# Optimization experiments

Hardware: AMD Instinct MI355X
Metric: run time of the kernel (lower is better)

Reference implementation:

```python
import jax, jax.numpy as jnp
import numpy as np

B, T, D_IN, D_OUT = 4, 2048, 1024, 1024

def setup_inputs() -> dict:
    key = jax.random.key(0)
    k1, k2, k3, k4 = jax.random.split(key, 4)
    scale = 0.02
    return {
        "x": jax.random.normal(k1, (B, T, D_IN), dtype=jnp.float32),
        "W_query": jax.random.normal(k2, (D_IN, D_OUT), dtype=jnp.float32) * scale,
        "W_key": jax.random.normal(k3, (D_IN, D_OUT), dtype=jnp.float32) * scale,
        "W_value": jax.random.normal(k4, (D_IN, D_OUT), dtype=jnp.float32) * scale,
    }

def reference(x, W_query, W_key, W_value):
    # QKV projections (Linear without bias)
    q = jnp.einsum("btd,de->bte", x, W_query)
    k = jnp.einsum("btd,de->bte", x, W_key)
    v = jnp.einsum("btd,de->bte", x, W_value)
    num_tokens = x.shape[1]
    d_out = k.shape[-1]
    # raw scores [B, T, T]
    scores = jnp.einsum("bqd,bkd->bqk", q, k)
    # causal mask: position q may attend to k <= q
    causal = jnp.tril(jnp.ones((num_tokens, num_tokens), dtype=bool))
    scores = jnp.where(causal, scores, -jnp.inf)
    attn = jax.nn.softmax(scores / jnp.sqrt(jnp.float32(d_out)), axis=-1)
    # dropout is identity at eval / p=0.0
    context = jnp.einsum("bqk,bkd->bqd", attn, v)
    return context
```

## Files before the change

kernel.cpp:

```cpp
#include <hip/hip_runtime.h>
#include <hip/hip_bf16.h>
#include <stdint.h>

typedef short short8 __attribute__((ext_vector_type(8)));
typedef short short4v __attribute__((ext_vector_type(4)));
typedef float f32x4 __attribute__((ext_vector_type(4)));

__device__ __forceinline__ void gload16(const void* g, void* l) {
  __builtin_amdgcn_global_load_lds((const __attribute__((address_space(1))) void*)g,
                                   (__attribute__((address_space(3))) void*)l, 16, 0, 0);
}

__device__ __forceinline__ unsigned short f2b(float f) {
  unsigned int x = __float_as_uint(f);
  x += 0x7fffu + ((x >> 16) & 1u);
  return (unsigned short)(x >> 16);
}

__global__ __launch_bounds__(256) void prep(
    const float* __restrict__ x, const float* __restrict__ Wq,
    const float* __restrict__ Wk, const float* __restrict__ Wv,
    unsigned short* __restrict__ xb, unsigned short* __restrict__ Wt2,
    float* __restrict__ sums)
{
  __shared__ __align__(16) char smem[16384];
  const int bid = blockIdx.x;
  const int tid = threadIdx.x;
  if (bid < 8192) {
    const int i = bid * 256 + tid;
    const float4 f = ((const float4*)x)[i];
    union { unsigned short u[4]; uint2 v; } o;
    o.u[0] = f2b(f.x); o.u[1] = f2b(f.y); o.u[2] = f2b(f.z); o.u[3] = f2b(f.w);
    ((uint2*)xb)[i] = o.v;
  } else if (bid < 9216) {
    float (*tb)[33] = (float(*)[33])smem;
    const int t = bid - 8192;
    const int bx = t & 31, by = t >> 5;
    const int tx = tid & 31, ty = tid >> 5;
    const int xcol = bx * 32 + tx, y0 = by * 32;
    #pragma unroll
    for (int i = 0; i < 4; ++i)
      tb[ty + i * 8][tx] = Wv[(long long)(y0 + ty + i * 8) * 1024 + xcol];
    __syncthreads();
    unsigned short* O = Wt2 + 1024 * 1024;
    const int xo = by * 32 + tx, yo0 = bx * 32;
    #pragma unroll
    for (int i = 0; i < 4; ++i)
      O[(long long)(yo0 + ty + i * 8) * 1024 + xo] = f2b(tb[tx][ty + i * 8]);
  } else if (bid < 9472) {
    const int t = bid - 9216;
    const int bx = t & 15, by = t >> 4;
    const int row0 = by * 64, col0 = bx * 64;
    const int wave = tid >> 6, lane = tid & 63;
    const int wr = wave >> 1, wc = wave & 1;
    const int l15 = lane & 15, lk = lane >> 4;
    const int sr = lane >> 3, sg = lane & 7;
    char* lA = smem;
    char* lB = smem + 8192;
    const int rA = wr * 32 + l15, cB = wc * 32 + l15;
    const int xorA = (rA & 7) << 4, xorB = (cB & 7) << 4;
    const int kb = lk * 16;
    f32x4 acc[2][2];
    #pragma unroll
    for (int m = 0; m < 2; ++m)
      #pragma unroll
      for (int n = 0; n < 2; ++n) acc[m][n] = (f32x4)0.0f;
    for (int kt = 0; kt < 16; ++kt) {
      const int kc = kt * 64;
      short8 va[2], vb[2];
      int rr[2];
      #pragma unroll
      for (int j = 0; j < 2; ++j) {
        const int ci = wave * 2 + j;
        const int r = ci * 8 + sr;
        rr[j] = r;
        const float* pa = Wk + (long long)(row0 + r) * 1024 + kc + sg * 8;
        const float* pb = Wq + (long long)(col0 + r) * 1024 + kc + sg * 8;
        const float4 a0 = *(const float4*)pa, a1 = *(const float4*)(pa + 4);
        const float4 b0 = *(const float4*)pb, b1 = *(const float4*)(pb + 4);
        va[j][0] = (short)f2b(a0.x); va[j][1] = (short)f2b(a0.y);
        va[j][2] = (short)f2b(a0.z); va[j][3] = (short)f2b(a0.w);
        va[j][4] = (short)f2b(a1.x); va[j][5] = (short)f2b(a1.y);
        va[j][6] = (short)f2b(a1.z); va[j][7] = (short)f2b(a1.w);
        vb[j][0] = (short)f2b(b0.x); vb[j][1] = (short)f2b(b0.y);
        vb[j][2] = (short)f2b(b0.z); vb[j][3] = (short)f2b(b0.w);
        vb[j][4] = (short)f2b(b1.x); vb[j][5] = (short)f2b(b1.y);
        vb[j][6] = (short)f2b(b1.z); vb[j][7] = (short)f2b(b1.w);
      }
      __syncthreads();
      #pragma unroll
      for (int j = 0; j < 2; ++j) {
        const int off = rr[j] * 128 + ((sg * 16) ^ ((rr[j] & 7) << 4));
        *(short8*)(lA + off) = va[j];
        *(short8*)(lB + off) = vb[j];
      }
      __syncthreads();
      #pragma unroll
      for (int ks = 0; ks < 2; ++ks) {
        short8 af[2], bf[2];
        #pragma unroll
        for (int m = 0; m < 2; ++m)
          af[m] = *(const short8*)(lA + (rA + m * 16) * 128 + ((ks * 64 + kb) ^ xorA));
        #pragma unroll
        for (int n = 0; n < 2; ++n)
          bf[n] = *(const short8*)(lB + (cB + n * 16) * 128 + ((ks * 64 + kb) ^ xorB));
        #pragma unroll
        for (int m = 0; m < 2; ++m)
          #pragma unroll
          for (int n = 0; n < 2; ++n)
            acc[m][n] = __builtin_amdgcn_mfma_f32_16x16x32_bf16(af[m], bf[n], acc[m][n], 0, 0, 0);
      }
    }
    const int orow = row0 + wr * 32 + lk * 4;
    const int ocol = col0 + wc * 32 + l15;
    #pragma unroll
    for (int m = 0; m < 2; ++m)
      #pragma unroll
      for (int r = 0; r < 4; ++r)
        #pragma unroll
        for (int n = 0; n < 2; ++n)
          Wt2[(long long)(orow + m * 16 + r) * 1024 + ocol + n * 16] = f2b(acc[m][n][r]);
  } else {
    const int i = (bid - 9472) * 256 + tid;
    sums[i] = 0.f;
  }
}

#define STG(buf, isB, half, kt) do {                                           \
    const unsigned short* _s = (isB) ? Bz : Az;                                \
    const int _ld = (isB) ? ldb : lda;                                         \
    const int _b0 = (isB) ? col0 : row0;                                       \
    char* _d = lds + (buf) * 65536 + (isB) * 32768 + (half) * 16384;           \
    _Pragma("unroll")                                                          \
    for (int _i = 0; _i < 2; ++_i) {                                           \
      const int _c = wave * 2 + _i;                                            \
      const int _row = (half) * 128 + _c * 8 + srow;                           \
      gload16(_s + (long long)(_b0 + _row) * _ld + (kt) * 64 + sgrp * 8,       \
              _d + _c * 1024);                                                 \
    } } while (0)

#define LDA8(dst, buf, mh) do {                                                \
    _Pragma("unroll")                                                          \
    for (int _m = 0; _m < 4; ++_m) {                                           \
      const int _r = wr * 128 + ((mh) * 4 + _m) * 16 + (lane & 15);            \
      const char* _p = lds + (buf) * 65536 + _r * 128;                         \
      const int _x = (_r & 7) << 4;                                            \
      dst[_m][0] = *(const short8*)(_p + ((kbyte) ^ _x));                      \
      dst[_m][1] = *(const short8*)(_p + ((64 + kbyte) ^ _x));                 \
    } } while (0)

#define LDB4(dst, buf, nh) do {                                                \
    _Pragma("unroll")                                                          \
    for (int _n = 0; _n < 2; ++_n) {                                           \
      const int _r = wc * 64 + ((nh) * 2 + _n) * 16 + (lane & 15);             \
      const char* _p = lds + (buf) * 65536 + 32768 + _r * 128;                 \
      const int _x = (_r & 7) << 4;                                            \
      dst[_n][0] = *(const short8*)(_p + ((kbyte) ^ _x));                      \
      dst[_n][1] = *(const short8*)(_p + ((64 + kbyte) ^ _x));                 \
    } } while (0)

#define MFMA16(mh, nh, av, bv) do {                                            \
    __builtin_amdgcn_s_setprio(1);                                             \
    _Pragma("unroll") for (int _n = 0; _n < 2; ++_n)                           \
    _Pragma("unroll") for (int _m = 0; _m < 4; ++_m)                           \
    _Pragma("unroll") for (int _k = 0; _k < 2; ++_k)                           \
      acc[(mh)*4+_m][(nh)*2+_n] = __builtin_amdgcn_mfma_f32_16x16x32_bf16(     \
          av[_m][_k], bv[_n][_k], acc[(mh)*4+_m][(nh)*2+_n], 0, 0, 0);         \
    __builtin_amdgcn_s_setprio(0);                                             \
  } while (0)

#define BAR() __builtin_amdgcn_s_barrier()
#define VM4() asm volatile("s_waitcnt vmcnt(4)" ::: "memory")
#define VM0() asm volatile("s_waitcnt vmcnt(0)" ::: "memory")

#define GEMM8_BODY(NT)                                                         \
  f32x4 acc[8][4];                                                             \
  _Pragma("unroll")                                                            \
  for (int m = 0; m < 8; ++m)                                                  \
    _Pragma("unroll")                                                          \
    for (int n = 0; n < 4; ++n) acc[m][n] = (f32x4)0.0f;                       \
  short8 a[4][2], b0[2][2], b1[2][2];                                          \
  STG(0, 1, 0, 0); STG(0, 1, 1, 0); STG(0, 0, 0, 0); STG(0, 0, 1, 0);          \
  STG(1, 1, 0, 1); STG(1, 1, 1, 1);                                            \
  VM4(); BAR();                                                                \
  for (int t = 0; t < (NT); ++t) {                                             \
    const bool pf = (t < (NT) - 1);                                            \
    LDA8(a, 0, 0); LDB4(b0, 0, 0);                                             \
    STG(1, 0, 0, 2 * t + 1);                                                   \
    BAR(); MFMA16(0, 0, a, b0); BAR();                                         \
    LDB4(b1, 0, 1);                                                            \
    STG(1, 0, 1, 2 * t + 1);                                                   \
    BAR(); MFMA16(0, 1, a, b1); BAR();                                         \
    LDA8(a, 0, 1);                                                             \
    if (pf) STG(0, 1, 0, 2 * t + 2);                                           \
    BAR(); MFMA16(1, 1, a, b1); BAR();                                         \
    if (pf) STG(0, 1, 1, 2 * t + 2);                                           \
    BAR(); MFMA16(1, 0, a, b0);                                                \
    if (pf) VM4(); else VM0();                                                 \
    BAR();                                                                     \
    LDA8(a, 1, 0); LDB4(b0, 1, 0);                                             \
    if (pf) STG(0, 0, 0, 2 * t + 2);                                           \
    BAR(); MFMA16(0, 0, a, b0); BAR();                                         \
    LDB4(b1, 1, 1);                                                            \
    if (pf) STG(0, 0, 1, 2 * t + 2);                                           \
    BAR(); MFMA16(0, 1, a, b1); BAR();                                         \
    LDA8(a, 1, 1);                                                             \
    if (pf) STG(1, 1, 0, 2 * t + 3);                                           \
    BAR(); MFMA16(1, 1, a, b1); BAR();                                         \
    if (pf) STG(1, 1, 1, 2 * t + 3);                                           \
    BAR(); MFMA16(1, 0, a, b0);                                                \
    if (pf) VM4();                                                             \
    BAR();                                                                     \
  }

__global__ __launch_bounds__(512, 2) void gemm8_yv(
    const unsigned short* __restrict__ A, const unsigned short* __restrict__ Bt,
    unsigned short* __restrict__ y, unsigned short* __restrict__ vt)
{
  const int row0 = blockIdx.y * 256;
  const int col0 = blockIdx.x * 256;
  const unsigned short* Az = A;
  const unsigned short* Bz = Bt;
  const int lda = 1024, ldb = 1024;

  __shared__ __align__(16) char lds[131072];

  const int tid = threadIdx.x;
  const int wave = tid >> 6, lane = tid & 63;
  const int wr = wave >> 2, wc = wave & 3;
  const int srow = lane >> 3, sgrp = (lane & 7) ^ srow;
  const int kbyte = (lane >> 4) * 16;

  GEMM8_BODY(8)

  const int orow = row0 + wr * 128 + ((lane >> 4) << 2);
  const int ocol = col0 + wc * 64 + (lane & 15);
  if (col0 < 1024) {
    #pragma unroll
    for (int m = 0; m < 8; ++m)
      #pragma unroll
      for (int r = 0; r < 4; ++r) {
        const int rg = orow + m * 16 + r;
        #pragma unroll
        for (int n = 0; n < 4; ++n)
          y[(long long)rg * 1024 + ocol + n * 16] = f2b(acc[m][n][r]);
      }
  } else {
    const int b = row0 >> 11;
    const int t0 = (row0 & 2047) + wr * 128 + ((lane >> 4) << 2);
    const int d0 = (col0 - 1024) + wc * 64 + (lane & 15);
    #pragma unroll
    for (int n = 0; n < 4; ++n) {
      unsigned short* vrow = vt + ((long long)b * 1024 + d0 + n * 16) * 2048 + t0;
      #pragma unroll
      for (int m = 0; m < 8; ++m) {
        short4v v;
        v[0] = (short)f2b(acc[m][n][0]);
        v[1] = (short)f2b(acc[m][n][1]);
        v[2] = (short)f2b(acc[m][n][2]);
        v[3] = (short)f2b(acc[m][n][3]);
        *(short4v*)(vrow + m * 16) = v;
      }
    }
  }
}

__global__ __launch_bounds__(512, 2) void gemm8_p(
    const unsigned short* __restrict__ A, const unsigned short* __restrict__ Bt,
    unsigned short* __restrict__ outp, float* __restrict__ sums)
{
  const int z = blockIdx.z;
  const int row0 = blockIdx.y * 256;
  const int col0 = blockIdx.x * 256;
  if (col0 > row0 + 255) return;

  const unsigned short* Az = A + (long long)z * (2048 * 1024);
  const unsigned short* Bz = Bt + (long long)z * (2048 * 1024);
  const int lda = 1024, ldb = 1024;

  __shared__ __align__(16) char lds[131072];

  const int tid = threadIdx.x;
  const int wave = tid >> 6, lane = tid & 63;
  const int wr = wave >> 2, wc = wave & 3;
  const int srow = lane >> 3, sgrp = (lane & 7) ^ srow;
  const int kbyte = (lane >> 4) * 16;

  GEMM8_BODY(8)

  const int orow = row0 + wr * 128 + ((lane >> 4) << 2);
  const int ocol = col0 + wc * 64 + (lane & 15);
  unsigned short* out = outp + (long long)z * (2048 * 2048);
  #pragma unroll
  for (int m = 0; m < 8; ++m)
    #pragma unroll
    for (int r = 0; r < 4; ++r) {
      const int rg = orow + m * 16 + r;
      float rs = 0.f;
      #pragma unroll
      for (int n = 0; n < 4; ++n) {
        const int cg = ocol + n * 16;
        float p = (cg > rg) ? 0.0f : __expf(acc[m][n][r] * 0.03125f);
        rs += p;
        out[(long long)rg * 2048 + cg] = f2b(p);
      }
      #pragma unroll
      for (int off = 1; off < 16; off <<= 1) rs += __shfl_xor(rs, off);
      if ((lane & 15) == 0) atomicAdd(&sums[(long long)z * 2048 + rg], rs);
    }
}

__global__ __launch_bounds__(256) void gemm_pv(
    const unsigned short* __restrict__ P, const unsigned short* __restrict__ Vt,
    float* __restrict__ out, const float* __restrict__ sums)
{
  const int z = blockIdx.z;
  const int row0 = (15 - blockIdx.y) * 128;
  const int col0 = blockIdx.x * 128;

  const unsigned short* Az = P + (long long)z * (2048 * 2048);
  const unsigned short* Bz = Vt + (long long)z * (1024 * 2048);

  __shared__ __align__(16) char lds[32768];

  const int tid = threadIdx.x;
  const int wave = tid >> 6;
  const int lane = tid & 63;
  const int wr = wave >> 1, wc = wave & 1;
  const int l15 = lane & 15, lk = lane >> 4;

  const int srow = lane >> 3;
  const int sgrp = (lane & 7) ^ srow;

  const int rA = wr * 64 + l15;
  const int cB = wc * 64 + l15;
  const int kb = lk * 16;
  const int xorA = (rA & 7) << 4;
  const int xorB = (cB & 7) << 4;

  f32x4 acc[4][4];
  #pragma unroll
  for (int m = 0; m < 4; ++m)
    #pragma unroll
    for (int n = 0; n < 4; ++n) acc[m][n] = (f32x4)0.0f;

  const int nkt = (row0 + 128) >> 6;

  for (int kt = 0; kt < nkt; ++kt) {
    const int kc = kt * 64;
    #pragma unroll
    for (int i = 0; i < 4; ++i) {
      const int ci = wave * 4 + i;
      gload16(Az + (long long)(row0 + ci * 8 + srow) * 2048 + kc + sgrp * 8,
              lds + ci * 1024);
      gload16(Bz + (long long)(col0 + ci * 8 + srow) * 2048 + kc + sgrp * 8,
              lds + 16384 + ci * 1024);
    }
    __syncthreads();
    #pragma unroll
    for (int ks = 0; ks < 2; ++ks) {
      short8 af[4], bfr[4];
      #pragma unroll
      for (int m = 0; m < 4; ++m)
        af[m] = *(const short8*)(lds + (rA + m * 16) * 128 + ((ks * 64 + kb) ^ xorA));
      #pragma unroll
      for (int n = 0; n < 4; ++n)
        bfr[n] = *(const short8*)(lds + 16384 + (cB + n * 16) * 128 + ((ks * 64 + kb) ^ xorB));
      #pragma unroll
      for (int m = 0; m < 4; ++m)
        #pragma unroll
        for (int n = 0; n < 4; ++n)
          acc[m][n] = __builtin_amdgcn_mfma_f32_16x16x32_bf16(af[m], bfr[n], acc[m][n], 0, 0, 0);
    }
    __syncthreads();
  }

  const int orow = row0 + wr * 64 + lk * 4;
  const int ocol = col0 + wc * 64 + l15;
  const float* sz = sums + (long long)z * 2048;
  float* oz = out + (long long)z * (2048 * 1024);
  #pragma unroll
  for (int m = 0; m < 4; ++m)
    #pragma unroll
    for (int r = 0; r < 4; ++r) {
      const int rg = orow + m * 16 + r;
      const float iv = 1.0f / sz[rg];
      #pragma unroll
      for (int n = 0; n < 4; ++n)
        oz[(long long)rg * 1024 + ocol + n * 16] = acc[m][n][r] * iv;
    }
}

extern "C" void kernel_launch(void* const* d_in, const int* in_sizes, int n_in,
                              void* d_out, int out_size, void* d_ws, size_t ws_size,
                              hipStream_t stream) {
  (void)in_sizes; (void)n_in; (void)out_size; (void)ws_size;
  const float* x  = (const float*)d_in[0];
  const float* Wq = (const float*)d_in[1];
  const float* Wk = (const float*)d_in[2];
  const float* Wv = (const float*)d_in[3];
  float* out = (float*)d_out;

  char* ws = (char*)d_ws;
  unsigned short* xb  = (unsigned short*)(ws);
  unsigned short* Wt2 = (unsigned short*)(ws + 16777216);
  unsigned short* y   = (unsigned short*)(ws + 20971520);
  unsigned short* Vt  = (unsigned short*)(ws + 37748736);
  unsigned short* P   = (unsigned short*)(ws + 54525952);
  float*          sums = (float*)(ws + 88080384);

  prep<<<9504, 256, 0, stream>>>(x, Wq, Wk, Wv, xb, Wt2, sums);

  gemm8_yv<<<dim3(8, 32), 512, 0, stream>>>(xb, Wt2, y, Vt);

  gemm8_p<<<dim3(8, 8, 4), 512, 0, stream>>>(y, xb, P, sums);

  gemm_pv<<<dim3(8, 16, 4), 256, 0, stream>>>(P, Vt, out, sums);
}
```

Before: 156.7 us.

## Unify score and PV GEMMs into triangular-scheduled 256x128 kernel with split-K

Replaces the score GEMM and the PV GEMM with one templated 256x128-tile kernel. The score mode enumerates only lower-triangular tiles through a flattened index, so no blocks launch just to exit early. The PV mode splits the long K range of the bottom four row blocks into two halves that atomically add into the output, which is pre-zeroed for those rows by extra blocks in prep. This balances per-block work across the causal triangle and gives PV the deeper pipelined schedule, at the cost of float atomics, more prep work and narrower tiles.

```diff
diff --git a/kernel.cpp b/kernel.cpp
--- a/kernel.cpp
+++ b/kernel.cpp
@@ -21,7 +21,7 @@
     const float* __restrict__ x, const float* __restrict__ Wq,
     const float* __restrict__ Wk, const float* __restrict__ Wv,
     unsigned short* __restrict__ xb, unsigned short* __restrict__ Wt2,
-    float* __restrict__ sums)
+    float* __restrict__ sums, float* __restrict__ out)
 {
   __shared__ __align__(16) char smem[16384];
   const int bid = blockIdx.x;
@@ -120,9 +120,15 @@
         #pragma unroll
         for (int n = 0; n < 2; ++n)
           Wt2[(long long)(orow + m * 16 + r) * 1024 + ocol + n * 16] = f2b(acc[m][n][r]);
-  } else {
+  } else if (bid < 9504) {
     const int i = (bid - 9472) * 256 + tid;
     sums[i] = 0.f;
+  } else {
+    const long long i = (long long)(bid - 9504) * 256 + tid;
+    const int z = (int)(i >> 18);
+    const int r = (int)(i & 262143);
+    float4* p = (float4*)(out + (long long)z * 2097152 + 1048576) + r;
+    *p = make_float4(0.f, 0.f, 0.f, 0.f);
   }
 }
 
@@ -171,47 +177,8 @@
 
 #define BAR() __builtin_amdgcn_s_barrier()
 #define VM4() asm volatile("s_waitcnt vmcnt(4)" ::: "memory")
+#define VM2() asm volatile("s_waitcnt vmcnt(2)" ::: "memory")
 #define VM0() asm volatile("s_waitcnt vmcnt(0)" ::: "memory")
-
-#define GEMM8_BODY(NT)                                                         \
-  f32x4 acc[8][4];                                                             \
-  _Pragma("unroll")                                                            \
-  for (int m = 0; m < 8; ++m)                                                  \
-    _Pragma("unroll")                                                          \
-    for (int n = 0; n < 4; ++n) acc[m][n] = (f32x4)0.0f;                       \
-  short8 a[4][2], b0[2][2], b1[2][2];                                          \
-  STG(0, 1, 0, 0); STG(0, 1, 1, 0); STG(0, 0, 0, 0); STG(0, 0, 1, 0);          \
-  STG(1, 1, 0, 1); STG(1, 1, 1, 1);                                            \
-  VM4(); BAR();                                                                \
-  for (int t = 0; t < (NT); ++t) {                                             \
-    const bool pf = (t < (NT) - 1);                                            \
-    LDA8(a, 0, 0); LDB4(b0, 0, 0);                                             \
-    STG(1, 0, 0, 2 * t + 1);                                                   \
-    BAR(); MFMA16(0, 0, a, b0); BAR();                                         \
-    LDB4(b1, 0, 1);                                                            \
-    STG(1, 0, 1, 2 * t + 1);                                                   \
-    BAR(); MFMA16(0, 1, a, b1); BAR();                                         \
-    LDA8(a, 0, 1);                                                             \
-    if (pf) STG(0, 1, 0, 2 * t + 2);                                           \
-    BAR(); MFMA16(1, 1, a, b1); BAR();                                         \
-    if (pf) STG(0, 1, 1, 2 * t + 2);                                           \
-    BAR(); MFMA16(1, 0, a, b0);                                                \
-    if (pf) VM4(); else VM0();                                                 \
-    BAR();                                                                     \
-    LDA8(a, 1, 0); LDB4(b0, 1, 0);                                             \
-    if (pf) STG(0, 0, 0, 2 * t + 2);                                           \
-    BAR(); MFMA16(0, 0, a, b0); BAR();                                         \
-    LDB4(b1, 1, 1);                                                            \
-    if (pf) STG(0, 0, 1, 2 * t + 2);                                           \
-    BAR(); MFMA16(0, 1, a, b1); BAR();                                         \
-    LDA8(a, 1, 1);                                                             \
-    if (pf) STG(1, 1, 0, 2 * t + 3);                                           \
-    BAR(); MFMA16(1, 1, a, b1); BAR();                                         \
-    if (pf) STG(1, 1, 1, 2 * t + 3);                                           \
-    BAR(); MFMA16(1, 0, a, b0);                                                \
-    if (pf) VM4();                                                             \
-    BAR();                                                                     \
-  }
 
 __global__ __launch_bounds__(512, 2) void gemm8_yv(
     const unsigned short* __restrict__ A, const unsigned short* __restrict__ Bt,
@@ -230,8 +197,48 @@
   const int wr = wave >> 2, wc = wave & 3;
   const int srow = lane >> 3, sgrp = (lane & 7) ^ srow;
   const int kbyte = (lane >> 4) * 16;
-
-  GEMM8_BODY(8)
+  const int nt = 8;
+
+  f32x4 acc[8][4];
+  #pragma unroll
+  for (int m = 0; m < 8; ++m)
+    #pragma unroll
+    for (int n = 0; n < 4; ++n) acc[m][n] = (f32x4)0.0f;
+  short8 a[4][2], b0[2][2], b1[2][2];
+
+  STG(0, 1, 0, 0); STG(0, 1, 1, 0); STG(0, 0, 0, 0); STG(0, 0, 1, 0);
+  STG(1, 1, 0, 1); STG(1, 1, 1, 1);
+  VM4(); BAR();
+
+  for (int t = 0; t < nt; ++t) {
+    const bool pf = (t < nt - 1);
+    LDA8(a, 0, 0); LDB4(b0, 0, 0);
+    STG(1, 0, 0, 2 * t + 1);
+    BAR(); MFMA16(0, 0, a, b0); BAR();
+    LDB4(b1, 0, 1);
+    STG(1, 0, 1, 2 * t + 1);
+    BAR(); MFMA16(0, 1, a, b1); BAR();
+    LDA8(a, 0, 1);
+    if (pf) STG(0, 1, 0, 2 * t + 2);
+    BAR(); MFMA16(1, 1, a, b1); BAR();
+    if (pf) STG(0, 1, 1, 2 * t + 2);
+    BAR(); MFMA16(1, 0, a, b0);
+    if (pf) VM4(); else VM0();
+    BAR();
+    LDA8(a, 1, 0); LDB4(b0, 1, 0);
+    if (pf) STG(0, 0, 0, 2 * t + 2);
+    BAR(); MFMA16(0, 0, a, b0); BAR();
+    LDB4(b1, 1, 1);
+    if (pf) STG(0, 0, 1, 2 * t + 2);
+    BAR(); MFMA16(0, 1, a, b1); BAR();
+    LDA8(a, 1, 1);
+    if (pf) STG(1, 1, 0, 2 * t + 3);
+    BAR(); MFMA16(1, 1, a, b1); BAR();
+    if (pf) STG(1, 1, 1, 2 * t + 3);
+    BAR(); MFMA16(1, 0, a, b0);
+    if (pf) VM4();
+    BAR();
+  }
 
   const int orow = row0 + wr * 128 + ((lane >> 4) << 2);
   const int ocol = col0 + wc * 64 + (lane & 15);
@@ -265,20 +272,92 @@
   }
 }
 
-__global__ __launch_bounds__(512, 2) void gemm8_p(
-    const unsigned short* __restrict__ A, const unsigned short* __restrict__ Bt,
-    unsigned short* __restrict__ outp, float* __restrict__ sums)
+#define STGA2(buf, half, kt) do {                                              \
+    _Pragma("unroll")                                                          \
+    for (int _i = 0; _i < 2; ++_i) {                                           \
+      const int _c = wave * 2 + _i;                                            \
+      gload16(Az + (long long)(row0 + (half) * 128 + _c * 8 + srow) * lda +    \
+                  (kt) * 64 + sgrp * 8,                                        \
+              lds + (buf) * 32768 + (half) * 16384 + _c * 1024);               \
+    } } while (0)
+
+#define STGB2(buf, half, kt)                                                   \
+    gload16(Bz + (long long)(col0 + (half) * 64 + wave * 8 + srow) * ldb +     \
+                (kt) * 64 + sgrp * 8,                                          \
+            lds + 65536 + (buf) * 16384 + (half) * 8192 + wave * 1024)
+
+#define LDA8N(dst, buf, mh) do {                                               \
+    _Pragma("unroll")                                                          \
+    for (int _m = 0; _m < 4; ++_m) {                                           \
+      const int _r = wr * 128 + ((mh) * 4 + _m) * 16 + (lane & 15);            \
+      const char* _p = lds + (buf) * 32768 + _r * 128;                         \
+      const int _x = (_r & 7) << 4;                                            \
+      dst[_m][0] = *(const short8*)(_p + ((kbyte) ^ _x));                      \
+      dst[_m][1] = *(const short8*)(_p + ((64 + kbyte) ^ _x));                 \
+    } } while (0)
+
+#define LDB1N(dst, buf, nf) do {                                               \
+    const int _r = wc * 32 + (nf) * 16 + (lane & 15);                          \
+    const char* _p = lds + 65536 + (buf) * 16384 + _r * 128;                   \
+    const int _x = (_r & 7) << 4;                                              \
+    dst[0] = *(const short8*)(_p + ((kbyte) ^ _x));                            \
+    dst[1] = *(const short8*)(_p + ((64 + kbyte) ^ _x));                       \
+  } while (0)
+
+#define MFMA8N(mh, nf, av, bv) do {                                            \
+    __builtin_amdgcn_s_setprio(1);                                             \
+    _Pragma("unroll") for (int _m = 0; _m < 4; ++_m)                           \
+    _Pragma("unroll") for (int _k = 0; _k < 2; ++_k)                           \
+      acc[(mh)*4+_m][nf] = __builtin_amdgcn_mfma_f32_16x16x32_bf16(            \
+          av[_m][_k], bv[_k], acc[(mh)*4+_m][nf], 0, 0, 0);                    \
+    __builtin_amdgcn_s_setprio(0);                                             \
+  } while (0)
+
+template<int MODE>
+__global__ __launch_bounds__(512, 2) void gemm8n(
+    const unsigned short* __restrict__ Abase, const unsigned short* __restrict__ Bbase,
+    void* __restrict__ outv, float* __restrict__ sums)
 {
   const int z = blockIdx.z;
-  const int row0 = blockIdx.y * 256;
-  const int col0 = blockIdx.x * 256;
-  if (col0 > row0 + 255) return;
-
-  const unsigned short* Az = A + (long long)z * (2048 * 1024);
-  const unsigned short* Bz = Bt + (long long)z * (2048 * 1024);
-  const int lda = 1024, ldb = 1024;
-
-  __shared__ __align__(16) char lds[131072];
+  const int f = blockIdx.x;
+  int row0, col0, k0, nt;
+  bool atomic = false;
+  const unsigned short *Az, *Bz;
+  int lda, ldb;
+
+  if (MODE == 1) {
+    int by = (int)((sqrtf(4.f * f + 1.f) - 1.f) * 0.5f);
+    while (by * (by + 1) > f) --by;
+    while ((by + 1) * (by + 2) <= f) ++by;
+    const int bx = f - by * (by + 1);
+    row0 = by * 256; col0 = bx * 128; k0 = 0; nt = 8;
+    Az = Abase + (long long)z * (2048 * 1024);
+    Bz = Bbase + (long long)z * (2048 * 1024);
+    lda = 1024; ldb = 1024;
+  } else {
+    int by, bx;
+    if (f < 64) {
+      by = 7 - (f >> 4);
+      const int c = (f >> 3) & 1;
+      bx = f & 7;
+      k0 = c * 1024;
+      const int kEnd = 256 * (by + 1);
+      nt = ((c == 0 ? 1024 : kEnd - 1024) >> 7);
+      atomic = true;
+    } else {
+      const int g = f - 64;
+      by = 3 - (g >> 3);
+      bx = g & 7;
+      k0 = 0;
+      nt = (256 * (by + 1)) >> 7;
+    }
+    row0 = by * 256; col0 = bx * 128;
+    Az = Abase + (long long)z * (2048 * 2048) + k0;
+    Bz = Bbase + (long long)z * (1024 * 2048) + k0;
+    lda = 2048; ldb = 2048;
+  }
+
+  __shared__ __align__(16) char lds[98304];
 
   const int tid = threadIdx.x;
   const int wave = tid >> 6, lane = tid & 63;
@@ -286,109 +365,84 @@
   const int srow = lane >> 3, sgrp = (lane & 7) ^ srow;
   const int kbyte = (lane >> 4) * 16;
 
-  GEMM8_BODY(8)
+  f32x4 acc[8][2];
+  #pragma unroll
+  for (int m = 0; m < 8; ++m) { acc[m][0] = (f32x4)0.0f; acc[m][1] = (f32x4)0.0f; }
+  short8 a[4][2], b0[2], b1[2];
+
+  STGB2(0, 0, 0); STGB2(0, 1, 0); STGA2(0, 0, 0); STGA2(0, 1, 0);
+  STGB2(1, 0, 1); STGB2(1, 1, 1);
+  VM2(); BAR();
+
+  for (int t = 0; t < nt; ++t) {
+    const bool pf = (t < nt - 1);
+    LDA8N(a, 0, 0); LDB1N(b0, 0, 0);
+    STGA2(1, 0, 2 * t + 1);
+    BAR(); MFMA8N(0, 0, a, b0); BAR();
+    LDB1N(b1, 0, 1);
+    STGA2(1, 1, 2 * t + 1);
+    BAR(); MFMA8N(0, 1, a, b1); BAR();
+    LDA8N(a, 0, 1);
+    if (pf) STGB2(0, 0, 2 * t + 2);
+    BAR(); MFMA8N(1, 1, a, b1); BAR();
+    if (pf) STGB2(0, 1, 2 * t + 2);
+    BAR(); MFMA8N(1, 0, a, b0);
+    if (pf) VM2(); else VM0();
+    BAR();
+    LDA8N(a, 1, 0); LDB1N(b0, 1, 0);
+    if (pf) STGA2(0, 0, 2 * t + 2);
+    BAR(); MFMA8N(0, 0, a, b0); BAR();
+    LDB1N(b1, 1, 1);
+    if (pf) STGA2(0, 1, 2 * t + 2);
+    BAR(); MFMA8N(0, 1, a, b1); BAR();
+    LDA8N(a, 1, 1);
+    if (pf) STGB2(1, 0, 2 * t + 3);
+    BAR(); MFMA8N(1, 1, a, b1); BAR();
+    if (pf) STGB2(1, 1, 2 * t + 3);
+    BAR(); MFMA8N(1, 0, a, b0);
+    if (pf) VM2();
+    BAR();
+  }
 
   const int orow = row0 + wr * 128 + ((lane >> 4) << 2);
-  const int ocol = col0 + wc * 64 + (lane & 15);
-  unsigned short* out = outp + (long long)z * (2048 * 2048);
-  #pragma unroll
-  for (int m = 0; m < 8; ++m)
-    #pragma unroll
-    for (int r = 0; r < 4; ++r) {
-      const int rg = orow + m * 16 + r;
-      float rs = 0.f;
-      #pragma unroll
-      for (int n = 0; n < 4; ++n) {
-        const int cg = ocol + n * 16;
-        float p = (cg > rg) ? 0.0f : __expf(acc[m][n][r] * 0.03125f);
-        rs += p;
-        out[(long long)rg * 2048 + cg] = f2b(p);
-      }
-      #pragma unroll
-      for (int off = 1; off < 16; off <<= 1) rs += __shfl_xor(rs, off);
-      if ((lane & 15) == 0) atomicAdd(&sums[(long long)z * 2048 + rg], rs);
-    }
-}
-
-__global__ __launch_bounds__(256) void gemm_pv(
-    const unsigned short* __restrict__ P, const unsigned short* __restrict__ Vt,
-    float* __restrict__ out, const float* __restrict__ sums)
-{
-  const int z = blockIdx.z;
-  const int row0 = (15 - blockIdx.y) * 128;
-  const int col0 = blockIdx.x * 128;
-
-  const unsigned short* Az = P + (long long)z * (2048 * 2048);
-  const unsigned short* Bz = Vt + (long long)z * (1024 * 2048);
-
-  __shared__ __align__(16) char lds[32768];
-
-  const int tid = threadIdx.x;
-  const int wave = tid >> 6;
-  const int lane = tid & 63;
-  const int wr = wave >> 1, wc = wave & 1;
-  const int l15 = lane & 15, lk = lane >> 4;
-
-  const int srow = lane >> 3;
-  const int sgrp = (lane & 7) ^ srow;
-
-  const int rA = wr * 64 + l15;
-  const int cB = wc * 64 + l15;
-  const int kb = lk * 16;
-  const int xorA = (rA & 7) << 4;
-  const int xorB = (cB & 7) << 4;
-
-  f32x4 acc[4][4];
-  #pragma unroll
-  for (int m = 0; m < 4; ++m)
-    #pragma unroll
-    for (int n = 0; n < 4; ++n) acc[m][n] = (f32x4)0.0f;
-
-  const int nkt = (row0 + 128) >> 6;
-
-  for (int kt = 0; kt < nkt; ++kt) {
-    const int kc = kt * 64;
-    #pragma unroll
-    for (int i = 0; i < 4; ++i) {
-      const int ci = wave * 4 + i;
-      gload16(Az + (long long)(row0 + ci * 8 + srow) * 2048 + kc + sgrp * 8,
-              lds + ci * 1024);
-      gload16(Bz + (long long)(col0 + ci * 8 + srow) * 2048 + kc + sgrp * 8,
-              lds + 16384 + ci * 1024);
-    }
-    __syncthreads();
-    #pragma unroll
-    for (int ks = 0; ks < 2; ++ks) {
-      short8 af[4], bfr[4];
-      #pragma unroll
-      for (int m = 0; m < 4; ++m)
-        af[m] = *(const short8*)(lds + (rA + m * 16) * 128 + ((ks * 64 + kb) ^ xorA));
-      #pragma unroll
-      for (int n = 0; n < 4; ++n)
-        bfr[n] = *(const short8*)(lds + 16384 + (cB + n * 16) * 128 + ((ks * 64 + kb) ^ xorB));
-      #pragma unroll
-      for (int m = 0; m < 4; ++m)
-        #pragma unroll
-        for (int n = 0; n < 4; ++n)
-          acc[m][n] = __builtin_amdgcn_mfma_f32_16x16x32_bf16(af[m], bfr[n], acc[m][n], 0, 0, 0);
-    }
-    __syncthreads();
-  }
-
-  const int orow = row0 + wr * 64 + lk * 4;
-  const int ocol = col0 + wc * 64 + l15;
-  const float* sz = sums + (long long)z * 2048;
-  float* oz = out + (long long)z * (2048 * 1024);
-  #pragma unroll
-  for (int m = 0; m < 4; ++m)
-    #pragma unroll
-    for (int r = 0; r < 4; ++r) {
-      const int rg = orow + m * 16 + r;
-      const float iv = 1.0f / sz[rg];
-      #pragma unroll
-      for (int n = 0; n < 4; ++n)
-        oz[(long long)rg * 1024 + ocol + n * 16] = acc[m][n][r] * iv;
-    }
+  const int ocol = col0 + wc * 32 + (lane & 15);
+  if (MODE == 1) {
+    unsigned short* out = (unsigned short*)outv + (long long)z * (2048 * 2048);
+    #pragma unroll
+    for (int m = 0; m < 8; ++m)
+      #pragma unroll
+      for (int r = 0; r < 4; ++r) {
+        const int rg = orow + m * 16 + r;
+        float rs = 0.f;
+        #pragma unroll
+        for (int n = 0; n < 2; ++n) {
+          const int cg = ocol + n * 16;
+          float p = (cg > rg) ? 0.0f : __expf(acc[m][n][r] * 0.03125f);
+          rs += p;
+          out[(long long)rg * 2048 + cg] = f2b(p);
+        }
+        #pragma unroll
+        for (int off = 1; off < 16; off <<= 1) rs += __shfl_xor(rs, off);
+        if ((lane & 15) == 0) atomicAdd(&sums[(long long)z * 2048 + rg], rs);
+      }
+  } else {
+    float* oz = (float*)outv + (long long)z * (2048 * 1024);
+    const float* sz = sums + (long long)z * 2048;
+    #pragma unroll
+    for (int m = 0; m < 8; ++m)
+      #pragma unroll
+      for (int r = 0; r < 4; ++r) {
+        const int rg = orow + m * 16 + r;
+        const float iv = 1.0f / sz[rg];
+        #pragma unroll
+        for (int n = 0; n < 2; ++n) {
+          float* p = oz + (long long)rg * 1024 + ocol + n * 16;
+          const float val = acc[m][n][r] * iv;
+          if (atomic) atomicAdd(p, val);
+          else *p = val;
+        }
+      }
+  }
 }
 
 extern "C" void kernel_launch(void* const* d_in, const int* in_sizes, int n_in,
@@ -409,11 +463,11 @@
   unsigned short* P   = (unsigned short*)(ws + 54525952);
   float*          sums = (float*)(ws + 88080384);
 
-  prep<<<9504, 256, 0, stream>>>(x, Wq, Wk, Wv, xb, Wt2, sums);
+  prep<<<13600, 256, 0, stream>>>(x, Wq, Wk, Wv, xb, Wt2, sums, out);
 
   gemm8_yv<<<dim3(8, 32), 512, 0, stream>>>(xb, Wt2, y, Vt);
 
-  gemm8_p<<<dim3(8, 8, 4), 512, 0, stream>>>(y, xb, P, sums);
-
-  gemm_pv<<<dim3(8, 16, 4), 256, 0, stream>>>(P, Vt, out, sums);
-}
+  gemm8n<1><<<dim3(72, 1, 4), 512, 0, stream>>>(y, xb, P, sums);
+
+  gemm8n<2><<<dim3(96, 1, 4), 512, 0, stream>>>(P, Vt, out, sums);
+}
```

Result: slower. 192.1 us (+22.6%).

## Split-K the causal PV GEMM for lower row blocks to balance work

Applied to the files above, without the earlier changes.

Row blocks in the lower half of the causal P·V product now split their K range into two 1024-wide chunks handled by separate workgroups, which combine results with atomicAdd into the output. The prep kernel gets extra blocks that zero the affected output half so the atomics start from zero. This targets the load imbalance and tail effect where the longest causal rows dominate gemm_pv runtime. The cost is float atomics to global memory, extra zeroing traffic, and some launched blocks that exit immediately.

```diff
diff --git a/kernel.cpp b/kernel.cpp
--- a/kernel.cpp
+++ b/kernel.cpp
@@ -21,7 +21,7 @@
     const float* __restrict__ x, const float* __restrict__ Wq,
     const float* __restrict__ Wk, const float* __restrict__ Wv,
     unsigned short* __restrict__ xb, unsigned short* __restrict__ Wt2,
-    float* __restrict__ sums)
+    float* __restrict__ sums, float* __restrict__ out)
 {
   __shared__ __align__(16) char smem[16384];
   const int bid = blockIdx.x;
@@ -120,9 +120,15 @@
         #pragma unroll
         for (int n = 0; n < 2; ++n)
           Wt2[(long long)(orow + m * 16 + r) * 1024 + ocol + n * 16] = f2b(acc[m][n][r]);
-  } else {
+  } else if (bid < 9504) {
     const int i = (bid - 9472) * 256 + tid;
     sums[i] = 0.f;
+  } else {
+    const long long i = (long long)(bid - 9504) * 256 + tid;
+    const int z = (int)(i >> 18);
+    const int r = (int)(i & 262143);
+    float4* p = (float4*)(out + (long long)z * 2097152 + 1048576) + r;
+    *p = make_float4(0.f, 0.f, 0.f, 0.f);
   }
 }
 
@@ -315,11 +321,20 @@
     float* __restrict__ out, const float* __restrict__ sums)
 {
   const int z = blockIdx.z;
-  const int row0 = (15 - blockIdx.y) * 128;
+  const int q = blockIdx.y >> 1;
+  const int by = 15 - q;
+  const int c = blockIdx.y & 1;
+  const int nch = (by >= 8) ? 2 : 1;
+  if (c >= nch) return;
+  const int row0 = by * 128;
   const int col0 = blockIdx.x * 128;
-
-  const unsigned short* Az = P + (long long)z * (2048 * 2048);
-  const unsigned short* Bz = Vt + (long long)z * (1024 * 2048);
+  const int k0 = c * 1024;
+  const int kEnd = min(row0 + 128, k0 + 1024);
+  const int nkt = (kEnd - k0) >> 6;
+  const bool atom = (nch > 1);
+
+  const unsigned short* Az = P + (long long)z * (2048 * 2048) + k0;
+  const unsigned short* Bz = Vt + (long long)z * (1024 * 2048) + k0;
 
   __shared__ __align__(16) char lds[32768];
 
@@ -343,8 +358,6 @@
   for (int m = 0; m < 4; ++m)
     #pragma unroll
     for (int n = 0; n < 4; ++n) acc[m][n] = (f32x4)0.0f;
-
-  const int nkt = (row0 + 128) >> 6;
 
   for (int kt = 0; kt < nkt; ++kt) {
     const int kc = kt * 64;
@@ -386,8 +399,12 @@
       const int rg = orow + m * 16 + r;
       const float iv = 1.0f / sz[rg];
       #pragma unroll
-      for (int n = 0; n < 4; ++n)
-        oz[(long long)rg * 1024 + ocol + n * 16] = acc[m][n][r] * iv;
+      for (int n = 0; n < 4; ++n) {
+        float* p = oz + (long long)rg * 1024 + ocol + n * 16;
+        const float val = acc[m][n][r] * iv;
+        if (atom) atomicAdd(p, val);
+        else *p = val;
+      }
     }
 }
 
@@ -409,11 +426,11 @@
   unsigned short* P   = (unsigned short*)(ws + 54525952);
   float*          sums = (float*)(ws + 88080384);
 
-  prep<<<9504, 256, 0, stream>>>(x, Wq, Wk, Wv, xb, Wt2, sums);
+  prep<<<13600, 256, 0, stream>>>(x, Wq, Wk, Wv, xb, Wt2, sums, out);
 
   gemm8_yv<<<dim3(8, 32), 512, 0, stream>>>(xb, Wt2, y, Vt);
 
   gemm8_p<<<dim3(8, 8, 4), 512, 0, stream>>>(y, xb, P, sums);
 
-  gemm_pv<<<dim3(8, 16, 4), 256, 0, stream>>>(P, Vt, out, sums);
-}
+  gemm_pv<<<dim3(8, 32, 4), 256, 0, stream>>>(P, Vt, out, sums);
+}
```

After: 162.6 us. 3.8% more time.
